# Optimization experiments

Hardware: AMD Instinct MI355X
Metric: run time of the kernel (lower is better)

## Reference

```python
import jax, jax.numpy as jnp
import numpy as np

HEAD_DIM = 128
HIDDEN = 2048
MAX_SEQ = 2048
NUM_HEADS = 16
NUM_KV_HEADS = 8
NUM_LAYERS = 32
LAYER_IDX = 5
SCALE = 1.0 / HEAD_DIM ** 0.5
N_REP = NUM_HEADS // NUM_KV_HEADS


def setup_inputs() -> dict:
    key = jax.random.key(0)
    ks = jax.random.split(key, 6)
    x = jax.random.normal(ks[0], (1, HIDDEN, 1, 1), jnp.float32)
    kv_cache = jax.random.normal(ks[1], (2 * NUM_LAYERS, NUM_KV_HEADS, MAX_SEQ, HEAD_DIM), jnp.float32)
    q_w = jax.random.normal(ks[2], (NUM_HEADS * HEAD_DIM, HIDDEN), jnp.float32) * 0.02
    k_w = jax.random.normal(ks[3], (NUM_KV_HEADS * HEAD_DIM, HIDDEN), jnp.float32) * 0.02
    v_w = jax.random.normal(ks[4], (NUM_KV_HEADS * HEAD_DIM, HIDDEN), jnp.float32) * 0.02
    o_w = jax.random.normal(ks[5], (HIDDEN, NUM_HEADS * HEAD_DIM), jnp.float32) * 0.02
    return {"x": x, "kv_cache": kv_cache, "q_w": q_w, "k_w": k_w, "v_w": v_w,
            "o_w": o_w, "current_pos": 1024}


def reference(x, kv_cache, q_w, k_w, v_w, o_w, current_pos):
    # 1x1 Conv2d on [1, C, 1, 1] == matrix-vector product
    xv = x.reshape(HIDDEN)
    q = (q_w @ xv).reshape(NUM_HEADS, HEAD_DIM)        # [H, D]
    k = (k_w @ xv).reshape(NUM_KV_HEADS, HEAD_DIM)     # [KV, D]
    v = (v_w @ xv).reshape(NUM_KV_HEADS, HEAD_DIM)     # [KV, D]

    k_idx = 2 * LAYER_IDX
    v_idx = k_idx + 1
    # functional slice-write of the new token's K/V into the cache
    kv_cache = kv_cache.at[k_idx, :, current_pos, :].set(k)
    kv_cache = kv_cache.at[v_idx, :, current_pos, :].set(v)

    k_full = kv_cache[k_idx]   # [KV, S, D]
    v_full = kv_cache[v_idx]   # [KV, S, D]

    # GQA: q head h uses kv head h // N_REP (matches repeat+view in torch)
    qg = q.reshape(NUM_KV_HEADS, N_REP, HEAD_DIM)                     # [KV, R, D]
    scores = jnp.einsum('grd,gsd->grs', qg, k_full) * SCALE           # [KV, R, S]
    probs = jax.nn.softmax(scores, axis=-1)
    attn = jnp.einsum('grs,gsd->grd', probs, v_full)                  # [KV, R, D]
    attn = attn.reshape(NUM_HEADS * HEAD_DIM)

    out = (o_w @ attn).reshape(1, HIDDEN, 1, 1)
    return out
```

## Files before the change

### kernel.cpp

```cpp
#include <hip/hip_runtime.h>

#define HEAD_DIM   128
#define HIDDEN     2048
#define MAX_SEQ    2048
#define NUM_HEADS  16
#define NUM_KV     8
#define LAYER_IDX  5
#define NSPLIT     64
#define CHUNK      (MAX_SEQ / NSPLIT)
#define SCALE      0.08838834764831845f

#define WS_Q     0
#define WS_K     2048
#define WS_V     3072
#define WS_M     4096
#define WS_L     5120
#define WS_O     6144
#define WS_ATTN  137216

__device__ __forceinline__ float wave_reduce_sum(float v) {
    #pragma unroll
    for (int off = 32; off > 0; off >>= 1) v += __shfl_xor(v, off);
    return v;
}

__global__ __launch_bounds__(256) void qkv_kernel(const float* __restrict__ x,
                                                  const float* __restrict__ q_w,
                                                  const float* __restrict__ k_w,
                                                  const float* __restrict__ v_w,
                                                  float* __restrict__ ws) {
    const int row = blockIdx.x;
    const float* w;
    float* out;
    if (row < 2048)      { w = q_w + (size_t)row * HIDDEN;          out = ws + WS_Q + row; }
    else if (row < 3072) { w = k_w + (size_t)(row - 2048) * HIDDEN; out = ws + WS_K + (row - 2048); }
    else                 { w = v_w + (size_t)(row - 3072) * HIDDEN; out = ws + WS_V + (row - 3072); }
    const int t = threadIdx.x;
    float4 a0 = ((const float4*)w)[t];
    float4 a1 = ((const float4*)w)[t + 256];
    float4 x0 = ((const float4*)x)[t];
    float4 x1 = ((const float4*)x)[t + 256];
    float p = a0.x * x0.x + a0.y * x0.y + a0.z * x0.z + a0.w * x0.w
            + a1.x * x1.x + a1.y * x1.y + a1.z * x1.z + a1.w * x1.w;
    p = wave_reduce_sum(p);
    __shared__ float red[4];
    if ((t & 63) == 0) red[t >> 6] = p;
    __syncthreads();
    if (t == 0) *out = red[0] + red[1] + red[2] + red[3];
}

__global__ __launch_bounds__(256) void attn_partial_kernel(const float* __restrict__ kv_cache,
                                                           const float* __restrict__ ws_qkv,
                                                           const int* __restrict__ cur_pos,
                                                           float* __restrict__ m_part,
                                                           float* __restrict__ l_part,
                                                           float* __restrict__ o_part) {
    const int g     = blockIdx.x;
    const int split = blockIdx.y;
    const int s0    = split * CHUNK;
    const int cpos  = *cur_pos;
    const int t     = threadIdx.x;
    const int wave  = t >> 6, lane = t & 63;

    const float* kbase = kv_cache + ((size_t)(2 * LAYER_IDX)     * NUM_KV + g) * (size_t)MAX_SEQ * HEAD_DIM;
    const float* vbase = kv_cache + ((size_t)(2 * LAYER_IDX + 1) * NUM_KV + g) * (size_t)MAX_SEQ * HEAD_DIM;
    const float* knew  = ws_qkv + WS_K + g * HEAD_DIM;
    const float* vnew  = ws_qkv + WS_V + g * HEAD_DIM;
    const float* q0    = ws_qkv + WS_Q + (g * 2 + 0) * HEAD_DIM;
    const float* q1    = ws_qkv + WS_Q + (g * 2 + 1) * HEAD_DIM;

    __shared__ float sc[2][CHUNK];
    __shared__ float ee[2][CHUNK];
    __shared__ float ml[2][2];

    float2 q0v = *(const float2*)(q0 + lane * 2);
    float2 q1v = *(const float2*)(q1 + lane * 2);
    #pragma unroll
    for (int i = 0; i < CHUNK / 4; ++i) {
        int j = wave * (CHUNK / 4) + i;
        int s = s0 + j;
        const float* krow = (s == cpos) ? knew : (kbase + (size_t)s * HEAD_DIM);
        float2 kk = *(const float2*)(krow + lane * 2);
        float d0 = q0v.x * kk.x + q0v.y * kk.y;
        float d1 = q1v.x * kk.x + q1v.y * kk.y;
        d0 = wave_reduce_sum(d0);
        d1 = wave_reduce_sum(d1);
        if (lane == 0) { sc[0][j] = d0 * SCALE; sc[1][j] = d1 * SCALE; }
    }
    __syncthreads();

    if (t < 2) {
        float m = -1e30f;
        for (int j = 0; j < CHUNK; ++j) m = fmaxf(m, sc[t][j]);
        float l = 0.f;
        for (int j = 0; j < CHUNK; ++j) { float e = __expf(sc[t][j] - m); ee[t][j] = e; l += e; }
        ml[t][0] = m; ml[t][1] = l;
    }
    __syncthreads();

    const int rep = t >> 7, d = t & 127;
    float acc = 0.f;
    #pragma unroll 4
    for (int j = 0; j < CHUNK; ++j) {
        int s = s0 + j;
        const float* vrow = (s == cpos) ? vnew : (vbase + (size_t)s * HEAD_DIM);
        acc += ee[rep][j] * vrow[d];
    }
    const int h = g * 2 + rep;
    o_part[((size_t)h * NSPLIT + split) * HEAD_DIM + d] = acc;
    if (d == 0) {
        m_part[h * NSPLIT + split] = ml[rep][0];
        l_part[h * NSPLIT + split] = ml[rep][1];
    }
}

__global__ __launch_bounds__(128) void combine_kernel(const float* __restrict__ m_part,
                                                      const float* __restrict__ l_part,
                                                      const float* __restrict__ o_part,
                                                      float* __restrict__ attn) {
    const int h = blockIdx.x;
    const int t = threadIdx.x;
    __shared__ float wsc[NSPLIT];
    __shared__ float Linv_s;
    if (t < 64) {
        float m = m_part[h * NSPLIT + t];
        float M = m;
        #pragma unroll
        for (int off = 32; off > 0; off >>= 1) M = fmaxf(M, __shfl_xor(M, off));
        float w = __expf(m - M);
        wsc[t] = w;
        float L = wave_reduce_sum(l_part[h * NSPLIT + t] * w);
        if (t == 0) Linv_s = 1.0f / L;
    }
    __syncthreads();
    float acc = 0.f;
    #pragma unroll 8
    for (int i = 0; i < NSPLIT; ++i)
        acc += o_part[((size_t)h * NSPLIT + i) * HEAD_DIM + t] * wsc[i];
    attn[h * HEAD_DIM + t] = acc * Linv_s;
}

__global__ __launch_bounds__(256) void out_kernel(const float* __restrict__ o_w,
                                                  const float* __restrict__ attn,
                                                  float* __restrict__ out) {
    const int row = blockIdx.x;
    const float* w = o_w + (size_t)row * HIDDEN;
    const int t = threadIdx.x;
    float4 a0 = ((const float4*)w)[t];
    float4 a1 = ((const float4*)w)[t + 256];
    float4 x0 = ((const float4*)attn)[t];
    float4 x1 = ((const float4*)attn)[t + 256];
    float p = a0.x * x0.x + a0.y * x0.y + a0.z * x0.z + a0.w * x0.w
            + a1.x * x1.x + a1.y * x1.y + a1.z * x1.z + a1.w * x1.w;
    p = wave_reduce_sum(p);
    __shared__ float red[4];
    if ((t & 63) == 0) red[t >> 6] = p;
    __syncthreads();
    if (t == 0) out[row] = red[0] + red[1] + red[2] + red[3];
}

extern "C" void kernel_launch(void* const* d_in, const int* in_sizes, int n_in,
                              void* d_out, int out_size, void* d_ws, size_t ws_size,
                              hipStream_t stream) {
    const float* x    = (const float*)d_in[0];
    const float* kv   = (const float*)d_in[1];
    const float* q_w  = (const float*)d_in[2];
    const float* k_w  = (const float*)d_in[3];
    const float* v_w  = (const float*)d_in[4];
    const float* o_w  = (const float*)d_in[5];
    const int*   cpos = (const int*)d_in[6];
    float* ws  = (float*)d_ws;
    float* out = (float*)d_out;

    qkv_kernel<<<4096, 256, 0, stream>>>(x, q_w, k_w, v_w, ws);
    attn_partial_kernel<<<dim3(NUM_KV, NSPLIT), 256, 0, stream>>>(
        kv, ws, cpos, ws + WS_M, ws + WS_L, ws + WS_O);
    combine_kernel<<<NUM_HEADS, 128, 0, stream>>>(ws + WS_M, ws + WS_L, ws + WS_O, ws + WS_ATTN);
    out_kernel<<<HIDDEN, 256, 0, stream>>>(o_w, ws + WS_ATTN, out);
}
```

Baseline: 29.37 us.

## Fuse split-KV combine into attention via atomic counter, batch GEMV rows per block

```diff
diff --git a/kernel.cpp b/kernel.cpp
--- a/kernel.cpp
+++ b/kernel.cpp
@@ -17,10 +17,21 @@
 #define WS_L     5120
 #define WS_O     6144
 #define WS_ATTN  137216
+#define WS_CNT   139264
 
 __device__ __forceinline__ float wave_reduce_sum(float v) {
     #pragma unroll
     for (int off = 32; off > 0; off >>= 1) v += __shfl_xor(v, off);
+    return v;
+}
+__device__ __forceinline__ float group32_reduce_sum(float v) {
+    #pragma unroll
+    for (int off = 16; off > 0; off >>= 1) v += __shfl_xor(v, off);
+    return v;
+}
+__device__ __forceinline__ float group32_reduce_max(float v) {
+    #pragma unroll
+    for (int off = 16; off > 0; off >>= 1) v = fmaxf(v, __shfl_xor(v, off));
     return v;
 }
 
@@ -28,33 +39,55 @@
                                                   const float* __restrict__ q_w,
                                                   const float* __restrict__ k_w,
                                                   const float* __restrict__ v_w,
-                                                  float* __restrict__ ws) {
-    const int row = blockIdx.x;
-    const float* w;
-    float* out;
-    if (row < 2048)      { w = q_w + (size_t)row * HIDDEN;          out = ws + WS_Q + row; }
-    else if (row < 3072) { w = k_w + (size_t)(row - 2048) * HIDDEN; out = ws + WS_K + (row - 2048); }
-    else                 { w = v_w + (size_t)(row - 3072) * HIDDEN; out = ws + WS_V + (row - 3072); }
+                                                  float* __restrict__ ws,
+                                                  unsigned int* __restrict__ cnt) {
     const int t = threadIdx.x;
-    float4 a0 = ((const float4*)w)[t];
-    float4 a1 = ((const float4*)w)[t + 256];
+    if (blockIdx.x == 0 && t < NUM_KV) cnt[t] = 0u;
+
     float4 x0 = ((const float4*)x)[t];
     float4 x1 = ((const float4*)x)[t + 256];
-    float p = a0.x * x0.x + a0.y * x0.y + a0.z * x0.z + a0.w * x0.w
-            + a1.x * x1.x + a1.y * x1.y + a1.z * x1.z + a1.w * x1.w;
-    p = wave_reduce_sum(p);
-    __shared__ float red[4];
-    if ((t & 63) == 0) red[t >> 6] = p;
-    __syncthreads();
-    if (t == 0) *out = red[0] + red[1] + red[2] + red[3];
-}
-
-__global__ __launch_bounds__(256) void attn_partial_kernel(const float* __restrict__ kv_cache,
-                                                           const float* __restrict__ ws_qkv,
-                                                           const int* __restrict__ cur_pos,
-                                                           float* __restrict__ m_part,
-                                                           float* __restrict__ l_part,
-                                                           float* __restrict__ o_part) {
+    const int row0 = blockIdx.x * 8;
+
+    float p[8];
+    #pragma unroll
+    for (int r = 0; r < 8; ++r) {
+        const int row = row0 + r;
+        const float* w;
+        if (row < 2048)      w = q_w + (size_t)row * HIDDEN;
+        else if (row < 3072) w = k_w + (size_t)(row - 2048) * HIDDEN;
+        else                 w = v_w + (size_t)(row - 3072) * HIDDEN;
+        float4 a0 = ((const float4*)w)[t];
+        float4 a1 = ((const float4*)w)[t + 256];
+        p[r] = a0.x * x0.x + a0.y * x0.y + a0.z * x0.z + a0.w * x0.w
+             + a1.x * x1.x + a1.y * x1.y + a1.z * x1.z + a1.w * x1.w;
+    }
+    #pragma unroll
+    for (int r = 0; r < 8; ++r) p[r] = wave_reduce_sum(p[r]);
+
+    __shared__ float red[8][4];
+    const int wave = t >> 6, lane = t & 63;
+    if (lane == 0) {
+        #pragma unroll
+        for (int r = 0; r < 8; ++r) red[r][wave] = p[r];
+    }
+    __syncthreads();
+    if (t < 8) {
+        const int row = row0 + t;
+        float v = red[t][0] + red[t][1] + red[t][2] + red[t][3];
+        if (row < 2048)      ws[WS_Q + row] = v * SCALE;
+        else if (row < 3072) ws[WS_K + (row - 2048)] = v;
+        else                 ws[WS_V + (row - 3072)] = v;
+    }
+}
+
+__global__ __launch_bounds__(256) void attn_kernel(const float* __restrict__ kv_cache,
+                                                   const float* __restrict__ wsq,
+                                                   const int* __restrict__ cur_pos,
+                                                   float* __restrict__ m_part,
+                                                   float* __restrict__ l_part,
+                                                   float* __restrict__ o_part,
+                                                   float* __restrict__ attn,
+                                                   unsigned int* __restrict__ cnt) {
     const int g     = blockIdx.x;
     const int split = blockIdx.y;
     const int s0    = split * CHUNK;
@@ -64,99 +97,160 @@
 
     const float* kbase = kv_cache + ((size_t)(2 * LAYER_IDX)     * NUM_KV + g) * (size_t)MAX_SEQ * HEAD_DIM;
     const float* vbase = kv_cache + ((size_t)(2 * LAYER_IDX + 1) * NUM_KV + g) * (size_t)MAX_SEQ * HEAD_DIM;
-    const float* knew  = ws_qkv + WS_K + g * HEAD_DIM;
-    const float* vnew  = ws_qkv + WS_V + g * HEAD_DIM;
-    const float* q0    = ws_qkv + WS_Q + (g * 2 + 0) * HEAD_DIM;
-    const float* q1    = ws_qkv + WS_Q + (g * 2 + 1) * HEAD_DIM;
-
-    __shared__ float sc[2][CHUNK];
-    __shared__ float ee[2][CHUNK];
-    __shared__ float ml[2][2];
+    const float* knew  = wsq + WS_K + g * HEAD_DIM;
+    const float* vnew  = wsq + WS_V + g * HEAD_DIM;
+    const float* q0    = wsq + WS_Q + (g * 2 + 0) * HEAD_DIM;
+    const float* q1    = wsq + WS_Q + (g * 2 + 1) * HEAD_DIM;
+
+    __shared__ float  sc[2][CHUNK];
+    __shared__ float  ee[2][CHUNK];
+    __shared__ float  ml[2][2];
+    __shared__ float4 smv[2][8][32];
+    __shared__ float  wsc[2][NSPLIT];
+    __shared__ float  linv[2];
+    __shared__ int    lastf;
 
     float2 q0v = *(const float2*)(q0 + lane * 2);
     float2 q1v = *(const float2*)(q1 + lane * 2);
     #pragma unroll
     for (int i = 0; i < CHUNK / 4; ++i) {
-        int j = wave * (CHUNK / 4) + i;
-        int s = s0 + j;
+        const int j = wave * (CHUNK / 4) + i;
+        const int s = s0 + j;
         const float* krow = (s == cpos) ? knew : (kbase + (size_t)s * HEAD_DIM);
         float2 kk = *(const float2*)(krow + lane * 2);
         float d0 = q0v.x * kk.x + q0v.y * kk.y;
         float d1 = q1v.x * kk.x + q1v.y * kk.y;
         d0 = wave_reduce_sum(d0);
         d1 = wave_reduce_sum(d1);
-        if (lane == 0) { sc[0][j] = d0 * SCALE; sc[1][j] = d1 * SCALE; }
-    }
-    __syncthreads();
-
-    if (t < 2) {
-        float m = -1e30f;
-        for (int j = 0; j < CHUNK; ++j) m = fmaxf(m, sc[t][j]);
-        float l = 0.f;
-        for (int j = 0; j < CHUNK; ++j) { float e = __expf(sc[t][j] - m); ee[t][j] = e; l += e; }
-        ml[t][0] = m; ml[t][1] = l;
-    }
-    __syncthreads();
-
-    const int rep = t >> 7, d = t & 127;
-    float acc = 0.f;
-    #pragma unroll 4
-    for (int j = 0; j < CHUNK; ++j) {
-        int s = s0 + j;
-        const float* vrow = (s == cpos) ? vnew : (vbase + (size_t)s * HEAD_DIM);
-        acc += ee[rep][j] * vrow[d];
-    }
-    const int h = g * 2 + rep;
-    o_part[((size_t)h * NSPLIT + split) * HEAD_DIM + d] = acc;
-    if (d == 0) {
-        m_part[h * NSPLIT + split] = ml[rep][0];
-        l_part[h * NSPLIT + split] = ml[rep][1];
-    }
-}
-
-__global__ __launch_bounds__(128) void combine_kernel(const float* __restrict__ m_part,
-                                                      const float* __restrict__ l_part,
-                                                      const float* __restrict__ o_part,
-                                                      float* __restrict__ attn) {
-    const int h = blockIdx.x;
-    const int t = threadIdx.x;
-    __shared__ float wsc[NSPLIT];
-    __shared__ float Linv_s;
+        if (lane == 0) { sc[0][j] = d0; sc[1][j] = d1; }
+    }
+    __syncthreads();
+
     if (t < 64) {
-        float m = m_part[h * NSPLIT + t];
+        const int rr = t >> 5, j = t & 31;
+        float v = sc[rr][j];
+        float m = group32_reduce_max(v);
+        float e = __expf(v - m);
+        ee[rr][j] = e;
+        float l = group32_reduce_sum(e);
+        if (j == 0) { ml[rr][0] = m; ml[rr][1] = l; }
+    }
+    __syncthreads();
+
+    {
+        const int rs = lane >> 5, q4 = lane & 31;
+        float4 a0 = {0.f, 0.f, 0.f, 0.f}, a1 = {0.f, 0.f, 0.f, 0.f};
+        #pragma unroll
+        for (int pass = 0; pass < 4; ++pass) {
+            const int j = pass * 8 + wave * 2 + rs;
+            const int s = s0 + j;
+            const float* vrow = (s == cpos) ? vnew : (vbase + (size_t)s * HEAD_DIM);
+            float4 vv = ((const float4*)vrow)[q4];
+            const float e0 = ee[0][j], e1 = ee[1][j];
+            a0.x += e0 * vv.x; a0.y += e0 * vv.y; a0.z += e0 * vv.z; a0.w += e0 * vv.w;
+            a1.x += e1 * vv.x; a1.y += e1 * vv.y; a1.z += e1 * vv.z; a1.w += e1 * vv.w;
+        }
+        smv[0][wave * 2 + rs][q4] = a0;
+        smv[1][wave * 2 + rs][q4] = a1;
+    }
+    __syncthreads();
+    if (t < 64) {
+        const int rep = t >> 5, q4 = t & 31;
+        float4 s = smv[rep][0][q4];
+        #pragma unroll
+        for (int r = 1; r < 8; ++r) {
+            float4 b = smv[rep][r][q4];
+            s.x += b.x; s.y += b.y; s.z += b.z; s.w += b.w;
+        }
+        const int h = g * 2 + rep;
+        ((float4*)(o_part + ((size_t)h * NSPLIT + split) * HEAD_DIM))[q4] = s;
+        if (q4 == 0) {
+            m_part[h * NSPLIT + split] = ml[rep][0];
+            l_part[h * NSPLIT + split] = ml[rep][1];
+        }
+    }
+    __syncthreads();
+
+    if (t == 0) {
+        __threadfence();
+        unsigned int old = atomicAdd(&cnt[g], 1u);
+        lastf = (old == NSPLIT - 1);
+    }
+    __syncthreads();
+    if (!lastf) return;
+    __threadfence();
+
+    if (t < 128) {
+        const int hh = t >> 6, i = t & 63;
+        const int h = g * 2 + hh;
+        float m = m_part[h * NSPLIT + i];
         float M = m;
         #pragma unroll
         for (int off = 32; off > 0; off >>= 1) M = fmaxf(M, __shfl_xor(M, off));
         float w = __expf(m - M);
-        wsc[t] = w;
-        float L = wave_reduce_sum(l_part[h * NSPLIT + t] * w);
-        if (t == 0) Linv_s = 1.0f / L;
-    }
-    __syncthreads();
-    float acc = 0.f;
-    #pragma unroll 8
-    for (int i = 0; i < NSPLIT; ++i)
-        acc += o_part[((size_t)h * NSPLIT + i) * HEAD_DIM + t] * wsc[i];
-    attn[h * HEAD_DIM + t] = acc * Linv_s;
+        wsc[hh][i] = w;
+        float l = wave_reduce_sum(l_part[h * NSPLIT + i] * w);
+        if (i == 0) linv[hh] = 1.0f / l;
+    }
+    __syncthreads();
+    {
+        const int hh = lane >> 5, q4 = lane & 31;
+        const int st = wave;
+        const int h = g * 2 + hh;
+        const float4* ob = (const float4*)(o_part + (size_t)h * NSPLIT * HEAD_DIM);
+        float4 acc = {0.f, 0.f, 0.f, 0.f};
+        #pragma unroll
+        for (int ii = 0; ii < 16; ++ii) {
+            const int i = st * 16 + ii;
+            const float w = wsc[hh][i];
+            float4 ov = ob[i * 32 + q4];
+            acc.x += w * ov.x; acc.y += w * ov.y; acc.z += w * ov.z; acc.w += w * ov.w;
+        }
+        float4* lred = (float4*)smv;
+        lred[st * 64 + lane] = acc;
+    }
+    __syncthreads();
+    if (t < 64) {
+        float4 s = ((float4*)smv)[lane];
+        #pragma unroll
+        for (int st = 1; st < 4; ++st) {
+            float4 b = ((float4*)smv)[st * 64 + lane];
+            s.x += b.x; s.y += b.y; s.z += b.z; s.w += b.w;
+        }
+        const float li = linv[lane >> 5];
+        s.x *= li; s.y *= li; s.z *= li; s.w *= li;
+        ((float4*)(attn + (size_t)(g * 2 + (lane >> 5)) * HEAD_DIM))[lane & 31] = s;
+    }
 }
 
 __global__ __launch_bounds__(256) void out_kernel(const float* __restrict__ o_w,
                                                   const float* __restrict__ attn,
                                                   float* __restrict__ out) {
-    const int row = blockIdx.x;
-    const float* w = o_w + (size_t)row * HIDDEN;
     const int t = threadIdx.x;
-    float4 a0 = ((const float4*)w)[t];
-    float4 a1 = ((const float4*)w)[t + 256];
     float4 x0 = ((const float4*)attn)[t];
     float4 x1 = ((const float4*)attn)[t + 256];
-    float p = a0.x * x0.x + a0.y * x0.y + a0.z * x0.z + a0.w * x0.w
-            + a1.x * x1.x + a1.y * x1.y + a1.z * x1.z + a1.w * x1.w;
-    p = wave_reduce_sum(p);
-    __shared__ float red[4];
-    if ((t & 63) == 0) red[t >> 6] = p;
-    __syncthreads();
-    if (t == 0) out[row] = red[0] + red[1] + red[2] + red[3];
+    const int row0 = blockIdx.x * 4;
+
+    float p[4];
+    #pragma unroll
+    for (int r = 0; r < 4; ++r) {
+        const float* w = o_w + (size_t)(row0 + r) * HIDDEN;
+        float4 a0 = ((const float4*)w)[t];
+        float4 a1 = ((const float4*)w)[t + 256];
+        p[r] = a0.x * x0.x + a0.y * x0.y + a0.z * x0.z + a0.w * x0.w
+             + a1.x * x1.x + a1.y * x1.y + a1.z * x1.z + a1.w * x1.w;
+    }
+    #pragma unroll
+    for (int r = 0; r < 4; ++r) p[r] = wave_reduce_sum(p[r]);
+
+    __shared__ float red[4][4];
+    const int wave = t >> 6, lane = t & 63;
+    if (lane == 0) {
+        #pragma unroll
+        for (int r = 0; r < 4; ++r) red[r][wave] = p[r];
+    }
+    __syncthreads();
+    if (t < 4) out[row0 + t] = red[t][0] + red[t][1] + red[t][2] + red[t][3];
 }
 
 extern "C" void kernel_launch(void* const* d_in, const int* in_sizes, int n_in,
@@ -171,10 +265,10 @@
     const int*   cpos = (const int*)d_in[6];
     float* ws  = (float*)d_ws;
     float* out = (float*)d_out;
-
-    qkv_kernel<<<4096, 256, 0, stream>>>(x, q_w, k_w, v_w, ws);
-    attn_partial_kernel<<<dim3(NUM_KV, NSPLIT), 256, 0, stream>>>(
-        kv, ws, cpos, ws + WS_M, ws + WS_L, ws + WS_O);
-    combine_kernel<<<NUM_HEADS, 128, 0, stream>>>(ws + WS_M, ws + WS_L, ws + WS_O, ws + WS_ATTN);
-    out_kernel<<<HIDDEN, 256, 0, stream>>>(o_w, ws + WS_ATTN, out);
-}
+    unsigned int* cnt = (unsigned int*)(ws + WS_CNT);
+
+    qkv_kernel<<<512, 256, 0, stream>>>(x, q_w, k_w, v_w, ws, cnt);
+    attn_kernel<<<dim3(NUM_KV, NSPLIT), 256, 0, stream>>>(
+        kv, ws, cpos, ws + WS_M, ws + WS_L, ws + WS_O, ws + WS_ATTN, cnt);
+    out_kernel<<<512, 256, 0, stream>>>(o_w, ws + WS_ATTN, out);
+}
```

Result: slower. 41.20 us (+40.3%).

## Fuse decode attention into one cooperative kernel with grid syncs

Applied to the files above, without the earlier changes.

```diff
diff --git a/kernel.cpp b/kernel.cpp
--- a/kernel.cpp
+++ b/kernel.cpp
@@ -1,4 +1,7 @@
 #include <hip/hip_runtime.h>
+#include <hip/hip_cooperative_groups.h>
+
+namespace cg = cooperative_groups;
 
 #define HEAD_DIM   128
 #define HIDDEN     2048
@@ -7,7 +10,7 @@
 #define NUM_KV     8
 #define LAYER_IDX  5
 #define NSPLIT     64
-#define CHUNK      (MAX_SEQ / NSPLIT)
+#define CHUNK      32
 #define SCALE      0.08838834764831845f
 
 #define WS_Q     0
@@ -23,140 +26,196 @@
     for (int off = 32; off > 0; off >>= 1) v += __shfl_xor(v, off);
     return v;
 }
-
-__global__ __launch_bounds__(256) void qkv_kernel(const float* __restrict__ x,
-                                                  const float* __restrict__ q_w,
-                                                  const float* __restrict__ k_w,
-                                                  const float* __restrict__ v_w,
-                                                  float* __restrict__ ws) {
-    const int row = blockIdx.x;
-    const float* w;
-    float* out;
-    if (row < 2048)      { w = q_w + (size_t)row * HIDDEN;          out = ws + WS_Q + row; }
-    else if (row < 3072) { w = k_w + (size_t)(row - 2048) * HIDDEN; out = ws + WS_K + (row - 2048); }
-    else                 { w = v_w + (size_t)(row - 3072) * HIDDEN; out = ws + WS_V + (row - 3072); }
-    const int t = threadIdx.x;
-    float4 a0 = ((const float4*)w)[t];
-    float4 a1 = ((const float4*)w)[t + 256];
-    float4 x0 = ((const float4*)x)[t];
-    float4 x1 = ((const float4*)x)[t + 256];
-    float p = a0.x * x0.x + a0.y * x0.y + a0.z * x0.z + a0.w * x0.w
-            + a1.x * x1.x + a1.y * x1.y + a1.z * x1.z + a1.w * x1.w;
-    p = wave_reduce_sum(p);
-    __shared__ float red[4];
-    if ((t & 63) == 0) red[t >> 6] = p;
-    __syncthreads();
-    if (t == 0) *out = red[0] + red[1] + red[2] + red[3];
-}
-
-__global__ __launch_bounds__(256) void attn_partial_kernel(const float* __restrict__ kv_cache,
-                                                           const float* __restrict__ ws_qkv,
-                                                           const int* __restrict__ cur_pos,
-                                                           float* __restrict__ m_part,
-                                                           float* __restrict__ l_part,
-                                                           float* __restrict__ o_part) {
-    const int g     = blockIdx.x;
-    const int split = blockIdx.y;
-    const int s0    = split * CHUNK;
-    const int cpos  = *cur_pos;
-    const int t     = threadIdx.x;
-    const int wave  = t >> 6, lane = t & 63;
-
-    const float* kbase = kv_cache + ((size_t)(2 * LAYER_IDX)     * NUM_KV + g) * (size_t)MAX_SEQ * HEAD_DIM;
-    const float* vbase = kv_cache + ((size_t)(2 * LAYER_IDX + 1) * NUM_KV + g) * (size_t)MAX_SEQ * HEAD_DIM;
-    const float* knew  = ws_qkv + WS_K + g * HEAD_DIM;
-    const float* vnew  = ws_qkv + WS_V + g * HEAD_DIM;
-    const float* q0    = ws_qkv + WS_Q + (g * 2 + 0) * HEAD_DIM;
-    const float* q1    = ws_qkv + WS_Q + (g * 2 + 1) * HEAD_DIM;
-
-    __shared__ float sc[2][CHUNK];
-    __shared__ float ee[2][CHUNK];
-    __shared__ float ml[2][2];
-
-    float2 q0v = *(const float2*)(q0 + lane * 2);
-    float2 q1v = *(const float2*)(q1 + lane * 2);
+__device__ __forceinline__ float group32_reduce_sum(float v) {
     #pragma unroll
-    for (int i = 0; i < CHUNK / 4; ++i) {
-        int j = wave * (CHUNK / 4) + i;
-        int s = s0 + j;
-        const float* krow = (s == cpos) ? knew : (kbase + (size_t)s * HEAD_DIM);
-        float2 kk = *(const float2*)(krow + lane * 2);
-        float d0 = q0v.x * kk.x + q0v.y * kk.y;
-        float d1 = q1v.x * kk.x + q1v.y * kk.y;
-        d0 = wave_reduce_sum(d0);
-        d1 = wave_reduce_sum(d1);
-        if (lane == 0) { sc[0][j] = d0 * SCALE; sc[1][j] = d1 * SCALE; }
-    }
-    __syncthreads();
-
-    if (t < 2) {
-        float m = -1e30f;
-        for (int j = 0; j < CHUNK; ++j) m = fmaxf(m, sc[t][j]);
-        float l = 0.f;
-        for (int j = 0; j < CHUNK; ++j) { float e = __expf(sc[t][j] - m); ee[t][j] = e; l += e; }
-        ml[t][0] = m; ml[t][1] = l;
-    }
-    __syncthreads();
-
-    const int rep = t >> 7, d = t & 127;
-    float acc = 0.f;
-    #pragma unroll 4
-    for (int j = 0; j < CHUNK; ++j) {
-        int s = s0 + j;
-        const float* vrow = (s == cpos) ? vnew : (vbase + (size_t)s * HEAD_DIM);
-        acc += ee[rep][j] * vrow[d];
-    }
-    const int h = g * 2 + rep;
-    o_part[((size_t)h * NSPLIT + split) * HEAD_DIM + d] = acc;
-    if (d == 0) {
-        m_part[h * NSPLIT + split] = ml[rep][0];
-        l_part[h * NSPLIT + split] = ml[rep][1];
-    }
-}
-
-__global__ __launch_bounds__(128) void combine_kernel(const float* __restrict__ m_part,
-                                                      const float* __restrict__ l_part,
-                                                      const float* __restrict__ o_part,
-                                                      float* __restrict__ attn) {
-    const int h = blockIdx.x;
-    const int t = threadIdx.x;
-    __shared__ float wsc[NSPLIT];
-    __shared__ float Linv_s;
-    if (t < 64) {
-        float m = m_part[h * NSPLIT + t];
-        float M = m;
-        #pragma unroll
-        for (int off = 32; off > 0; off >>= 1) M = fmaxf(M, __shfl_xor(M, off));
-        float w = __expf(m - M);
-        wsc[t] = w;
-        float L = wave_reduce_sum(l_part[h * NSPLIT + t] * w);
-        if (t == 0) Linv_s = 1.0f / L;
-    }
-    __syncthreads();
-    float acc = 0.f;
-    #pragma unroll 8
-    for (int i = 0; i < NSPLIT; ++i)
-        acc += o_part[((size_t)h * NSPLIT + i) * HEAD_DIM + t] * wsc[i];
-    attn[h * HEAD_DIM + t] = acc * Linv_s;
-}
-
-__global__ __launch_bounds__(256) void out_kernel(const float* __restrict__ o_w,
-                                                  const float* __restrict__ attn,
-                                                  float* __restrict__ out) {
-    const int row = blockIdx.x;
-    const float* w = o_w + (size_t)row * HIDDEN;
-    const int t = threadIdx.x;
-    float4 a0 = ((const float4*)w)[t];
-    float4 a1 = ((const float4*)w)[t + 256];
-    float4 x0 = ((const float4*)attn)[t];
-    float4 x1 = ((const float4*)attn)[t + 256];
-    float p = a0.x * x0.x + a0.y * x0.y + a0.z * x0.z + a0.w * x0.w
-            + a1.x * x1.x + a1.y * x1.y + a1.z * x1.z + a1.w * x1.w;
-    p = wave_reduce_sum(p);
-    __shared__ float red[4];
-    if ((t & 63) == 0) red[t >> 6] = p;
-    __syncthreads();
-    if (t == 0) out[row] = red[0] + red[1] + red[2] + red[3];
+    for (int off = 16; off > 0; off >>= 1) v += __shfl_xor(v, off);
+    return v;
+}
+__device__ __forceinline__ float group32_reduce_max(float v) {
+    #pragma unroll
+    for (int off = 16; off > 0; off >>= 1) v = fmaxf(v, __shfl_xor(v, off));
+    return v;
+}
+
+__global__ __launch_bounds__(512) void fused_decode_kernel(
+        const float* __restrict__ x,
+        const float* __restrict__ kv_cache,
+        const float* __restrict__ q_w,
+        const float* __restrict__ k_w,
+        const float* __restrict__ v_w,
+        const float* __restrict__ o_w,
+        const int*   __restrict__ cur_pos,
+        float* __restrict__ ws,
+        float* __restrict__ out) {
+    cg::grid_group grid = cg::this_grid();
+    const int t    = threadIdx.x;
+    const int wave = t >> 6, lane = t & 63;
+    const int b    = blockIdx.x;
+
+    __shared__ float  sc[2][2][CHUNK];
+    __shared__ float  ee[2][2][CHUNK];
+    __shared__ float  ml[2][2][2];
+    __shared__ float4 smv[2][2][8][32];
+    __shared__ float  wsc[NSPLIT];
+    __shared__ float  red4[4][HEAD_DIM];
+    __shared__ float  linv_s;
+
+    {
+        const int wg = b * 8 + wave;
+        const int r0 = wg * 2, r1 = r0 + 1;
+
+        float4 xv[8];
+        #pragma unroll
+        for (int k = 0; k < 8; ++k) xv[k] = ((const float4*)x)[lane + 64 * k];
+
+        const float *w0, *w1; float *o0, *o1; float s_out;
+        if (r0 < 2048) {
+            w0 = q_w + (size_t)r0 * HIDDEN;          w1 = q_w + (size_t)r1 * HIDDEN;
+            o0 = ws + WS_Q + r0;                      o1 = ws + WS_Q + r1;          s_out = SCALE;
+        } else if (r0 < 3072) {
+            w0 = k_w + (size_t)(r0 - 2048) * HIDDEN; w1 = k_w + (size_t)(r1 - 2048) * HIDDEN;
+            o0 = ws + WS_K + (r0 - 2048);             o1 = ws + WS_K + (r1 - 2048); s_out = 1.0f;
+        } else {
+            w0 = v_w + (size_t)(r0 - 3072) * HIDDEN; w1 = v_w + (size_t)(r1 - 3072) * HIDDEN;
+            o0 = ws + WS_V + (r0 - 3072);             o1 = ws + WS_V + (r1 - 3072); s_out = 1.0f;
+        }
+
+        float a0 = 0.f, a1 = 0.f;
+        #pragma unroll
+        for (int k = 0; k < 8; ++k) {
+            float4 wa = ((const float4*)w0)[lane + 64 * k];
+            float4 wb = ((const float4*)w1)[lane + 64 * k];
+            a0 += wa.x * xv[k].x + wa.y * xv[k].y + wa.z * xv[k].z + wa.w * xv[k].w;
+            a1 += wb.x * xv[k].x + wb.y * xv[k].y + wb.z * xv[k].z + wb.w * xv[k].w;
+        }
+        a0 = wave_reduce_sum(a0);
+        a1 = wave_reduce_sum(a1);
+        if (lane == 0) { *o0 = a0 * s_out; *o1 = a1 * s_out; }
+    }
+    grid.sync();
+
+    {
+        const int cpos  = *cur_pos;
+        const int p     = wave >> 2;
+        const int wl    = wave & 3;
+        const int pair  = b * 2 + p;
+        const int g     = pair >> 6;
+        const int split = pair & 63;
+        const int s0    = split * CHUNK;
+
+        const float* kbase = kv_cache + ((size_t)(2 * LAYER_IDX)     * NUM_KV + g) * (size_t)MAX_SEQ * HEAD_DIM;
+        const float* vbase = kv_cache + ((size_t)(2 * LAYER_IDX + 1) * NUM_KV + g) * (size_t)MAX_SEQ * HEAD_DIM;
+        const float* knew  = ws + WS_K + g * HEAD_DIM;
+        const float* vnew  = ws + WS_V + g * HEAD_DIM;
+        const float* q0    = ws + WS_Q + (g * 2 + 0) * HEAD_DIM;
+        const float* q1    = ws + WS_Q + (g * 2 + 1) * HEAD_DIM;
+
+        float2 q0v = *(const float2*)(q0 + lane * 2);
+        float2 q1v = *(const float2*)(q1 + lane * 2);
+        #pragma unroll
+        for (int i = 0; i < 8; ++i) {
+            const int j = wl * 8 + i;
+            const int s = s0 + j;
+            const float* krow = (s == cpos) ? knew : (kbase + (size_t)s * HEAD_DIM);
+            float2 kk = *(const float2*)(krow + lane * 2);
+            float d0 = q0v.x * kk.x + q0v.y * kk.y;
+            float d1 = q1v.x * kk.x + q1v.y * kk.y;
+            d0 = wave_reduce_sum(d0);
+            d1 = wave_reduce_sum(d1);
+            if (lane == 0) { sc[p][0][j] = d0; sc[p][1][j] = d1; }
+        }
+        __syncthreads();
+
+        if (wl == 0) {
+            const int rr = lane >> 5, j = lane & 31;
+            float v = sc[p][rr][j];
+            float m = group32_reduce_max(v);
+            float e = __expf(v - m);
+            ee[p][rr][j] = e;
+            float l = group32_reduce_sum(e);
+            if (j == 0) { ml[p][rr][0] = m; ml[p][rr][1] = l; }
+        }
+        __syncthreads();
+
+        {
+            const int rs = lane >> 5, q4 = lane & 31;
+            float4 a0 = {0.f, 0.f, 0.f, 0.f}, a1 = {0.f, 0.f, 0.f, 0.f};
+            #pragma unroll
+            for (int pass = 0; pass < 4; ++pass) {
+                const int j = pass * 8 + wl * 2 + rs;
+                const int s = s0 + j;
+                const float* vrow = (s == cpos) ? vnew : (vbase + (size_t)s * HEAD_DIM);
+                float4 vv = ((const float4*)vrow)[q4];
+                const float e0 = ee[p][0][j], e1 = ee[p][1][j];
+                a0.x += e0 * vv.x; a0.y += e0 * vv.y; a0.z += e0 * vv.z; a0.w += e0 * vv.w;
+                a1.x += e1 * vv.x; a1.y += e1 * vv.y; a1.z += e1 * vv.z; a1.w += e1 * vv.w;
+            }
+            smv[p][0][wl * 2 + rs][q4] = a0;
+            smv[p][1][wl * 2 + rs][q4] = a1;
+        }
+        __syncthreads();
+        if (wl == 0) {
+            const int rep = lane >> 5, q4 = lane & 31;
+            float4 s = smv[p][rep][0][q4];
+            #pragma unroll
+            for (int r = 1; r < 8; ++r) {
+                float4 bb = smv[p][rep][r][q4];
+                s.x += bb.x; s.y += bb.y; s.z += bb.z; s.w += bb.w;
+            }
+            const int h = g * 2 + rep;
+            ((float4*)(ws + WS_O + ((size_t)h * NSPLIT + split) * HEAD_DIM))[q4] = s;
+            if (q4 == 0) {
+                ws[WS_M + h * NSPLIT + split] = ml[p][rep][0];
+                ws[WS_L + h * NSPLIT + split] = ml[p][rep][1];
+            }
+        }
+    }
+    grid.sync();
+
+    if (b < NUM_HEADS) {
+        const int h = b;
+        if (t < 64) {
+            float m = ws[WS_M + h * NSPLIT + t];
+            float M = m;
+            #pragma unroll
+            for (int off = 32; off > 0; off >>= 1) M = fmaxf(M, __shfl_xor(M, off));
+            float w = __expf(m - M);
+            wsc[t] = w;
+            float L = wave_reduce_sum(ws[WS_L + h * NSPLIT + t] * w);
+            if (t == 0) linv_s = 1.0f / L;
+        }
+        __syncthreads();
+        {
+            const int d = t & 127, qtr = t >> 7;
+            float acc = 0.f;
+            #pragma unroll
+            for (int ii = 0; ii < 16; ++ii) {
+                const int i = qtr * 16 + ii;
+                acc += wsc[i] * ws[WS_O + ((size_t)h * NSPLIT + i) * HEAD_DIM + d];
+            }
+            red4[qtr][d] = acc;
+        }
+        __syncthreads();
+        if (t < 128)
+            ws[WS_ATTN + h * HEAD_DIM + t] =
+                (red4[0][t] + red4[1][t] + red4[2][t] + red4[3][t]) * linv_s;
+    }
+    grid.sync();
+
+    {
+        const int row = b * 8 + wave;
+        const float* w  = o_w + (size_t)row * HIDDEN;
+        const float* av = ws + WS_ATTN;
+        float acc = 0.f;
+        #pragma unroll
+        for (int k = 0; k < 8; ++k) {
+            float4 wa = ((const float4*)w)[lane + 64 * k];
+            float4 xa = ((const float4*)av)[lane + 64 * k];
+            acc += wa.x * xa.x + wa.y * xa.y + wa.z * xa.z + wa.w * xa.w;
+        }
+        acc = wave_reduce_sum(acc);
+        if (lane == 0) out[row] = acc;
+    }
 }
 
 extern "C" void kernel_launch(void* const* d_in, const int* in_sizes, int n_in,
@@ -172,9 +231,8 @@
     float* ws  = (float*)d_ws;
     float* out = (float*)d_out;
 
-    qkv_kernel<<<4096, 256, 0, stream>>>(x, q_w, k_w, v_w, ws);
-    attn_partial_kernel<<<dim3(NUM_KV, NSPLIT), 256, 0, stream>>>(
-        kv, ws, cpos, ws + WS_M, ws + WS_L, ws + WS_O);
-    combine_kernel<<<NUM_HEADS, 128, 0, stream>>>(ws + WS_M, ws + WS_L, ws + WS_O, ws + WS_ATTN);
-    out_kernel<<<HIDDEN, 256, 0, stream>>>(o_w, ws + WS_ATTN, out);
-}
+    void* args[] = { (void*)&x, (void*)&kv, (void*)&q_w, (void*)&k_w, (void*)&v_w,
+                     (void*)&o_w, (void*)&cpos, (void*)&ws, (void*)&out };
+    hipLaunchCooperativeKernel((void*)fused_decode_kernel, dim3(256), dim3(512),
+                               args, 0, stream);
+}
```

New measurement: 115.6 us. 294% more time.
